# Optimization experiments

Hardware: AMD Instinct MI355X
Metric: run time of the kernel (lower is better)

Reference implementation:

```python
import jax, jax.numpy as jnp
import numpy as np

HID = 1024
OUT = 512
BATCH = 512
SEQ = 128


def setup_inputs() -> dict:
    key = jax.random.key(0)
    ks = jax.random.split(key, 8)
    s = 1.0 / np.sqrt(HID)  # PyTorch LSTM/Linear init scale
    return {
        "C": jax.random.normal(ks[0], (BATCH, HID), jnp.float32),
        "t": jax.random.uniform(ks[1], (BATCH,), jnp.float32),
        "mask": jnp.ones((SEQ, BATCH), jnp.float32),
        "W_ih": jax.random.normal(ks[2], (4 * HID, HID), jnp.float32) * s,
        "W_hh": jax.random.normal(ks[3], (4 * HID, HID), jnp.float32) * s,
        "b_ih": jax.random.normal(ks[4], (4 * HID,), jnp.float32) * s,
        "b_hh": jax.random.normal(ks[5], (4 * HID,), jnp.float32) * s,
        "W_lin": jax.random.normal(ks[6], (OUT, HID), jnp.float32) * s,
        "b_lin": jax.random.normal(ks[7], (OUT,), jnp.float32) * s,
    }


def _lstm_scan(C, W_ih, W_hh, b_ih, b_hh, seq_len):
    # Input is the same C at every step -> precompute input projection once.
    x_proj = C @ W_ih.T + b_ih + b_hh  # [B, 4H]
    B, H = C.shape

    def step(carry, _):
        h, c = carry
        gates = x_proj + h @ W_hh.T  # [B, 4H]
        i, f, g, o = jnp.split(gates, 4, axis=-1)  # PyTorch gate order i,f,g,o
        i = jax.nn.sigmoid(i)
        f = jax.nn.sigmoid(f)
        g = jnp.tanh(g)
        o = jax.nn.sigmoid(o)
        c_new = f * c + i * g
        h_new = o * jnp.tanh(c_new)
        return (h_new, c_new), h_new

    h0 = jnp.zeros((B, H), C.dtype)
    c0 = jnp.zeros((B, H), C.dtype)
    _, hs = jax.lax.scan(step, (h0, c0), None, length=seq_len)
    return hs  # [T, B, H]


def reference(C, t, mask, W_ih, W_hh, b_ih, b_hh, W_lin, b_lin):
    # t and mask are unused in the original forward (t is shadowed, mask never read).
    hs = _lstm_scan(C, W_ih, W_hh, b_ih, b_hh, SEQ)  # [T, B, H]
    out = jnp.einsum("tbh,oh->tbo", hs, W_lin) + b_lin  # [T, B, O]
    return out
```

## Files before the change

kernel.cpp:

```cpp
#include <hip/hip_runtime.h>

#define B_   512
#define H_   1024
#define G4   4096
#define OUT_ 512
#define T_   128
#define APAD 72

typedef _Float16 h8  __attribute__((ext_vector_type(8)));
typedef _Float16 h4  __attribute__((ext_vector_type(4)));
typedef float    f32x4 __attribute__((ext_vector_type(4)));

#define MFMA16(a,b,c) __builtin_amdgcn_mfma_f32_16x16x32_f16(a,b,c,0,0,0)

__device__ __forceinline__ float sigmoidf_(float x) { return 1.f / (1.f + __expf(-x)); }

__global__ __launch_bounds__(256) void setup_kernel(
    const float* __restrict__ Wih, const float* __restrict__ Whh,
    const float* __restrict__ bih, const float* __restrict__ bhh,
    const float* __restrict__ Wlin,
    _Float16* __restrict__ Wih16, _Float16* __restrict__ Whh16,
    _Float16* __restrict__ Wlin16, float* __restrict__ bsum,
    float* __restrict__ cblob, _Float16* __restrict__ h0) {
  int i = blockIdx.x * blockDim.x + threadIdx.x;
  int stride = gridDim.x * blockDim.x;
  const f32x4* wih4 = (const f32x4*)Wih;
  const f32x4* whh4 = (const f32x4*)Whh;
  h4* wih16 = (h4*)Wih16;
  h4* whh16 = (h4*)Whh16;
  f32x4 z = {};
  for (int idx = i; idx < (G4 * H_) / 4; idx += stride) {
    f32x4 a = wih4[idx], b = whh4[idx];
    h4 va, vb;
#pragma unroll
    for (int r = 0; r < 4; ++r) { va[r] = (_Float16)a[r]; vb[r] = (_Float16)b[r]; }
    wih16[idx] = va; whh16[idx] = vb;
    if (idx < (OUT_ * H_) / 4) {
      f32x4 c = ((const f32x4*)Wlin)[idx];
      h4 vc;
#pragma unroll
      for (int r = 0; r < 4; ++r) vc[r] = (_Float16)c[r];
      ((h4*)Wlin16)[idx] = vc;
      ((f32x4*)cblob)[idx] = z;
    }
    if (idx < (B_ * H_ * 2) / 16)
      ((f32x4*)h0)[idx] = z;
    if (idx < G4 / 4)
      ((f32x4*)bsum)[idx] = ((const f32x4*)bih)[idx] + ((const f32x4*)bhh)[idx];
  }
}

__device__ __forceinline__ void proj_tile(int pid,
                                          const _Float16* __restrict__ h,
                                          const _Float16* __restrict__ Wlin16,
                                          const float* __restrict__ blin,
                                          float* __restrict__ outp,
                                          _Float16* smem) {
  int m0 = (pid >> 3) * 32, n0 = (pid & 7) * 64;
  int tid = threadIdx.x, w = tid >> 6, lane = tid & 63;
  _Float16* A_s = smem;
  _Float16* B_s = smem + 32 * APAD;
  f32x4 acc[2] = {};
  int fr_row = lane & 15, fr_k = (lane >> 4) * 8;
  int ar = tid >> 3, ac = (tid & 7) * 8;
  int br = tid >> 2, bq = (tid & 3) * 16;

  for (int kt = 0; kt < 16; ++kt) {
    int k0 = kt * 64;
    *(h8*)&A_s[ar * APAD + ac] = *(const h8*)(h + (size_t)(m0 + ar) * H_ + k0 + ac);
    const _Float16* bsrc = Wlin16 + (size_t)(n0 + br) * H_ + k0 + bq;
    *(h8*)&B_s[br * APAD + bq]     = *(const h8*)bsrc;
    *(h8*)&B_s[br * APAD + bq + 8] = *(const h8*)(bsrc + 8);
    __syncthreads();
#pragma unroll
    for (int s2 = 0; s2 < 2; ++s2) {
      int ks = s2 * 32 + fr_k;
      h8 a0 = *(const h8*)&A_s[fr_row * APAD + ks];
      h8 a1 = *(const h8*)&A_s[(16 + fr_row) * APAD + ks];
      h8 b  = *(const h8*)&B_s[(w * 16 + fr_row) * APAD + ks];
      acc[0] = MFMA16(a0, b, acc[0]);
      acc[1] = MFMA16(a1, b, acc[1]);
    }
    __syncthreads();
  }
  float* fr = (float*)smem + w * 512;
  float bl = blin[n0 + w * 16 + fr_row];
#pragma unroll
  for (int mf = 0; mf < 2; ++mf)
#pragma unroll
    for (int r = 0; r < 4; ++r)
      fr[((lane >> 4) * 4 + r + mf * 16) * 16 + fr_row] = acc[mf][r] + bl;
  __syncthreads();
  int row = lane >> 2, q = (lane & 3) * 4;
#pragma unroll
  for (int p = 0; p < 2; ++p) {
    f32x4 v = *(f32x4*)&fr[(row + p * 16) * 16 + q];
    *(f32x4*)(outp + (size_t)(m0 + row + p * 16) * OUT_ + n0 + w * 16 + q) = v;
  }
}

template <int IS_XPROJ>
__global__ __launch_bounds__(256) void gates_step_kernel(
    const void* __restrict__ Ag, const _Float16* __restrict__ Wg,
    const float* __restrict__ bsum, float* __restrict__ xblob,
    float* __restrict__ cblob, _Float16* __restrict__ hout,
    const _Float16* __restrict__ Wlin16, const float* __restrict__ blin,
    float* __restrict__ outp) {
  __shared__ __align__(16) _Float16 smem[64 * APAD + 128 * APAD];

  if (!IS_XPROJ && blockIdx.x >= 256) {
    proj_tile(blockIdx.x - 256, (const _Float16*)Ag, Wlin16, blin, outp, smem);
    return;
  }

  int blk = blockIdx.x;
  int xcd = blk & 7, kq = blk >> 3;
  int j_idx = xcd * 4 + (kq & 3), m_idx = kq >> 2;
  int m0 = m_idx * 64, j0 = j_idx * 32;
  int tid = threadIdx.x, w = tid >> 6, lane = tid & 63;
  int mhalf = w >> 1, jhalf = w & 1;
  _Float16* A_s = smem;
  _Float16* B_s = smem + 64 * APAD;
  f32x4 acc[4][2] = {};
  int fr_row = lane & 15, fr_k = (lane >> 4) * 8;
  int ar = tid >> 2, ac = (tid & 3) * 16;
  int r128 = tid >> 1, bg = r128 >> 5, brr = r128 & 31, bh = (tid & 1) * 32;
  const _Float16* Brow = Wg + (size_t)(bg * H_ + j0 + brr) * H_ + bh;

  for (int kt = 0; kt < 16; ++kt) {
    int k0 = kt * 64;
    if (IS_XPROJ) {
      const float* Af = (const float*)Ag;
      const f32x4* p = (const f32x4*)(Af + (size_t)(m0 + ar) * H_ + k0 + ac);
      f32x4 v0 = p[0], v1 = p[1], v2 = p[2], v3 = p[3];
      h8 hv0, hv1;
#pragma unroll
      for (int r = 0; r < 4; ++r) {
        hv0[r] = (_Float16)v0[r]; hv0[4 + r] = (_Float16)v1[r];
        hv1[r] = (_Float16)v2[r]; hv1[4 + r] = (_Float16)v3[r];
      }
      *(h8*)&A_s[ar * APAD + ac] = hv0;
      *(h8*)&A_s[ar * APAD + ac + 8] = hv1;
    } else {
      const _Float16* Ah = (const _Float16*)Ag;
      const h8* p = (const h8*)(Ah + (size_t)(m0 + ar) * H_ + k0 + ac);
      *(h8*)&A_s[ar * APAD + ac] = p[0];
      *(h8*)&A_s[ar * APAD + ac + 8] = p[1];
    }
    {
      const h8* src = (const h8*)(Brow + k0);
      _Float16* dst = &B_s[(bg * 32 + brr) * APAD + bh];
#pragma unroll
      for (int q = 0; q < 4; ++q) *(h8*)&dst[q * 8] = src[q];
    }
    __syncthreads();
#pragma unroll
    for (int s2 = 0; s2 < 2; ++s2) {
      int ks = s2 * 32 + fr_k;
      h8 a0 = *(const h8*)&A_s[(mhalf * 32 + fr_row) * APAD + ks];
      h8 a1 = *(const h8*)&A_s[(mhalf * 32 + 16 + fr_row) * APAD + ks];
#pragma unroll
      for (int g = 0; g < 4; ++g) {
        h8 b = *(const h8*)&B_s[(g * 32 + jhalf * 16 + fr_row) * APAD + ks];
        acc[g][0] = MFMA16(a0, b, acc[g][0]);
        acc[g][1] = MFMA16(a1, b, acc[g][1]);
      }
    }
    __syncthreads();
  }

  if (IS_XPROJ) {
    f32x4* xb = (f32x4*)xblob;
#pragma unroll
    for (int g = 0; g < 4; ++g) {
      float bs = bsum[g * H_ + j0 + jhalf * 16 + fr_row];
#pragma unroll
      for (int mf = 0; mf < 2; ++mf) {
        f32x4 v = acc[g][mf];
        v += bs;
        xb[(size_t)(blk * 32 + w * 8 + g * 2 + mf) * 64 + lane] = v;
      }
    }
  } else {
    f32x4* xb = (f32x4*)xblob;
    f32x4* cb = (f32x4*)cblob;
    _Float16* hr = smem + w * 512;
#pragma unroll
    for (int mf = 0; mf < 2; ++mf) {
      f32x4 xi = xb[(size_t)(blk * 32 + w * 8 + 0 + mf) * 64 + lane];
      f32x4 xf = xb[(size_t)(blk * 32 + w * 8 + 2 + mf) * 64 + lane];
      f32x4 xg = xb[(size_t)(blk * 32 + w * 8 + 4 + mf) * 64 + lane];
      f32x4 xo = xb[(size_t)(blk * 32 + w * 8 + 6 + mf) * 64 + lane];
      f32x4 cv = cb[(size_t)(blk * 8 + w * 2 + mf) * 64 + lane];
      f32x4 cn, hn;
#pragma unroll
      for (int r = 0; r < 4; ++r) {
        float iv = sigmoidf_(acc[0][mf][r] + xi[r]);
        float fv = sigmoidf_(acc[1][mf][r] + xf[r]);
        float gv = tanhf(acc[2][mf][r] + xg[r]);
        float ov = sigmoidf_(acc[3][mf][r] + xo[r]);
        float cc = fv * cv[r] + iv * gv;
        cn[r] = cc;
        hn[r] = ov * tanhf(cc);
      }
      cb[(size_t)(blk * 8 + w * 2 + mf) * 64 + lane] = cn;
#pragma unroll
      for (int r = 0; r < 4; ++r)
        hr[((lane >> 4) * 4 + r + mf * 16) * 16 + fr_row] = (_Float16)hn[r];
    }
    __syncthreads();
    int row = lane >> 1, hb2 = (lane & 1) * 8;
    h8 hv = *(const h8*)&hr[row * 16 + hb2];
    *(h8*)(hout + (size_t)(m0 + mhalf * 32 + row) * H_ + j0 + jhalf * 16 + hb2) = hv;
  }
}

__global__ __launch_bounds__(256) void proj_kernel(const _Float16* __restrict__ h,
                                                   const _Float16* __restrict__ Wlin16,
                                                   const float* __restrict__ blin,
                                                   float* __restrict__ outp) {
  __shared__ __align__(16) _Float16 smem[64 * APAD + 128 * APAD];
  proj_tile(blockIdx.x, h, Wlin16, blin, outp, smem);
}

extern "C" void kernel_launch(void* const* d_in, const int* in_sizes, int n_in,
                              void* d_out, int out_size, void* d_ws, size_t ws_size,
                              hipStream_t stream) {
  const float* C    = (const float*)d_in[0];
  const float* Wih  = (const float*)d_in[3];
  const float* Whh  = (const float*)d_in[4];
  const float* bih  = (const float*)d_in[5];
  const float* bhh  = (const float*)d_in[6];
  const float* Wlin = (const float*)d_in[7];
  const float* blin = (const float*)d_in[8];
  float* out = (float*)d_out;

  char* ws = (char*)d_ws;
  size_t off = 0;
  auto alloc = [&](size_t bytes) {
    void* p = ws + off;
    off = (off + bytes + 255) & ~(size_t)255;
    return p;
  };
  _Float16* Wih16  = (_Float16*)alloc((size_t)G4 * H_ * 2);
  _Float16* Whh16  = (_Float16*)alloc((size_t)G4 * H_ * 2);
  _Float16* Wlin16 = (_Float16*)alloc((size_t)OUT_ * H_ * 2);
  float*    bsum   = (float*)alloc((size_t)G4 * 4);
  float*    xblob  = (float*)alloc((size_t)B_ * G4 * 4);
  float*    cblob  = (float*)alloc((size_t)B_ * H_ * 4);
  _Float16* hb0    = (_Float16*)alloc((size_t)B_ * H_ * 2);
  _Float16* hb1    = (_Float16*)alloc((size_t)B_ * H_ * 2);
  if (off > ws_size) return;

  hipLaunchKernelGGL(setup_kernel, dim3(4096), dim3(256), 0, stream,
                     Wih, Whh, bih, bhh, Wlin, Wih16, Whh16, Wlin16, bsum, cblob, hb0);

  hipLaunchKernelGGL((gates_step_kernel<1>), dim3(256), dim3(256), 0, stream,
                     (const void*)C, Wih16, bsum, xblob, (float*)nullptr,
                     (_Float16*)nullptr, (const _Float16*)nullptr,
                     (const float*)nullptr, (float*)nullptr);

  _Float16* hb[2] = {hb0, hb1};
  for (int s = 1; s <= T_; ++s) {
    const _Float16* hin = hb[(s - 1) & 1];
    _Float16* ho = hb[s & 1];
    int grid = (s >= 2) ? 384 : 256;
    float* outp = (s >= 2) ? (out + (size_t)(s - 2) * B_ * OUT_) : out;
    hipLaunchKernelGGL((gates_step_kernel<0>), dim3(grid), dim3(256), 0, stream,
                       (const void*)hin, Whh16, bsum, xblob, cblob, ho, Wlin16, blin, outp);
  }
  hipLaunchKernelGGL(proj_kernel, dim3(128), dim3(256), 0, stream,
                     hb[0], Wlin16, blin, out + (size_t)(T_ - 1) * B_ * OUT_);
}
```

Baseline: 2.533 ms.

## Replace per-step launches with persistent LSTM kernel holding W_hh in LDS

Replaces the 128 per-timestep kernel launches with a single persistent kernel of 256 blocks. Each block keeps its fp16 slice of W_hh resident in 128KB of LDS and synchronises with the others through a flag-based global barrier after each step. The input projection is folded into the persistent kernel's prologue, c stays in registers, and all hidden states are written to a full history buffer. The output projection then runs afterwards as one large double-buffered GEMM. This removes launch overhead and repeated W_hh streaming, but it relies on all 256 blocks being co-resident (otherwise the barrier deadlocks). It also adds a fast rcp-based sigmoid/tanh and a larger workspace.

```diff
diff --git a/kernel.cpp b/kernel.cpp
--- a/kernel.cpp
+++ b/kernel.cpp
@@ -2,10 +2,11 @@
 
 #define B_   512
 #define H_   1024
-#define G4   4096
 #define OUT_ 512
 #define T_   128
 #define APAD 72
+#define BUFH (192 * APAD)
+#define BH_  ((size_t)B_ * H_)
 
 typedef _Float16 h8  __attribute__((ext_vector_type(8)));
 typedef _Float16 h4  __attribute__((ext_vector_type(4)));
@@ -13,214 +14,266 @@
 
 #define MFMA16(a,b,c) __builtin_amdgcn_mfma_f32_16x16x32_f16(a,b,c,0,0,0)
 
-__device__ __forceinline__ float sigmoidf_(float x) { return 1.f / (1.f + __expf(-x)); }
-
-__global__ __launch_bounds__(256) void setup_kernel(
-    const float* __restrict__ Wih, const float* __restrict__ Whh,
-    const float* __restrict__ bih, const float* __restrict__ bhh,
-    const float* __restrict__ Wlin,
-    _Float16* __restrict__ Wih16, _Float16* __restrict__ Whh16,
-    _Float16* __restrict__ Wlin16, float* __restrict__ bsum,
-    float* __restrict__ cblob, _Float16* __restrict__ h0) {
-  int i = blockIdx.x * blockDim.x + threadIdx.x;
-  int stride = gridDim.x * blockDim.x;
-  const f32x4* wih4 = (const f32x4*)Wih;
-  const f32x4* whh4 = (const f32x4*)Whh;
-  h4* wih16 = (h4*)Wih16;
-  h4* whh16 = (h4*)Whh16;
-  f32x4 z = {};
-  for (int idx = i; idx < (G4 * H_) / 4; idx += stride) {
-    f32x4 a = wih4[idx], b = whh4[idx];
-    h4 va, vb;
-#pragma unroll
-    for (int r = 0; r < 4; ++r) { va[r] = (_Float16)a[r]; vb[r] = (_Float16)b[r]; }
-    wih16[idx] = va; whh16[idx] = vb;
-    if (idx < (OUT_ * H_) / 4) {
-      f32x4 c = ((const f32x4*)Wlin)[idx];
-      h4 vc;
-#pragma unroll
-      for (int r = 0; r < 4; ++r) vc[r] = (_Float16)c[r];
-      ((h4*)Wlin16)[idx] = vc;
-      ((f32x4*)cblob)[idx] = z;
-    }
-    if (idx < (B_ * H_ * 2) / 16)
-      ((f32x4*)h0)[idx] = z;
-    if (idx < G4 / 4)
-      ((f32x4*)bsum)[idx] = ((const f32x4*)bih)[idx] + ((const f32x4*)bhh)[idx];
-  }
-}
-
-__device__ __forceinline__ void proj_tile(int pid,
-                                          const _Float16* __restrict__ h,
-                                          const _Float16* __restrict__ Wlin16,
-                                          const float* __restrict__ blin,
-                                          float* __restrict__ outp,
-                                          _Float16* smem) {
-  int m0 = (pid >> 3) * 32, n0 = (pid & 7) * 64;
+__device__ __forceinline__ float sigf_(float x) {
+  return __builtin_amdgcn_rcpf(1.f + __expf(-x));
+}
+__device__ __forceinline__ float tanhf_(float x) {
+  x = fmaxf(fminf(x, 20.f), -20.f);
+  float e = __expf(-2.f * x);
+  return (1.f - e) * __builtin_amdgcn_rcpf(1.f + e);
+}
+__device__ __forceinline__ h8 cvt8_(f32x4 lo, f32x4 hi) {
+  h8 r;
+#pragma unroll
+  for (int e = 0; e < 4; ++e) { r[e] = (_Float16)lo[e]; r[4 + e] = (_Float16)hi[e]; }
+  return r;
+}
+
+__global__ __launch_bounds__(256) void setup2_kernel(
+    const float* __restrict__ Wlin, _Float16* __restrict__ Wlin16,
+    _Float16* __restrict__ h0) {
+  int idx = blockIdx.x * 256 + threadIdx.x;
+  f32x4 v = ((const f32x4*)Wlin)[idx];
+  h4 o;
+#pragma unroll
+  for (int r = 0; r < 4; ++r) o[r] = (_Float16)v[r];
+  ((h4*)Wlin16)[idx] = o;
+  if (idx < 65536) ((f32x4*)h0)[idx] = (f32x4){0.f, 0.f, 0.f, 0.f};
+}
+
+__device__ __forceinline__ void gridbar_(unsigned* flags, unsigned* go, unsigned gen) {
+  __syncthreads();
+  if (threadIdx.x == 0) {
+    __threadfence();
+    __hip_atomic_store(&flags[blockIdx.x], gen, __ATOMIC_RELEASE, __HIP_MEMORY_SCOPE_AGENT);
+  }
+  if (blockIdx.x == 0) {
+    while (__hip_atomic_load(&flags[threadIdx.x], __ATOMIC_ACQUIRE, __HIP_MEMORY_SCOPE_AGENT) != gen)
+      __builtin_amdgcn_s_sleep(2);
+    __syncthreads();
+    if (threadIdx.x == 0)
+      __hip_atomic_store(go, gen, __ATOMIC_RELEASE, __HIP_MEMORY_SCOPE_AGENT);
+  }
+  if (threadIdx.x == 0) {
+    while (__hip_atomic_load(go, __ATOMIC_ACQUIRE, __HIP_MEMORY_SCOPE_AGENT) != gen)
+      __builtin_amdgcn_s_sleep(4);
+    __threadfence();
+  }
+  __syncthreads();
+}
+
+__global__ __launch_bounds__(256) void lstm_persistent_kernel(
+    const float* __restrict__ C,   const float* __restrict__ Whh,
+    const float* __restrict__ Wih, const float* __restrict__ bih,
+    const float* __restrict__ bhh, _Float16* __restrict__ hs,
+    unsigned* __restrict__ flags,  unsigned* __restrict__ go) {
+  __shared__ _Float16 Wlds[64 * H_];
+
+  const int blk  = blockIdx.x;
+  const int slab = blk >> 6;
+  const int j0   = (blk & 63) * 16;
+  const int m0   = slab * 128;
+  const int tid  = threadIdx.x, w = tid >> 6, lane = tid & 63;
+  const int col  = lane & 15;
+  const int khi  = lane >> 4;
+  const int xm   = (col & 7) << 4;
+
+  f32x4 acc[4][2];
+#pragma unroll
+  for (int g = 0; g < 4; ++g) { acc[g][0] = (f32x4){0.f,0.f,0.f,0.f}; acc[g][1] = (f32x4){0.f,0.f,0.f,0.f}; }
+
+  {
+    const float* aC0 = C + (size_t)(m0 + w * 32 + col) * H_ + khi * 8;
+    const float* aC1 = aC0 + 16 * H_;
+    const float* bW0 = Wih + (size_t)(0 * H_ + j0 + col) * H_ + khi * 8;
+    const float* bW1 = Wih + (size_t)(1 * H_ + j0 + col) * H_ + khi * 8;
+    const float* bW2 = Wih + (size_t)(2 * H_ + j0 + col) * H_ + khi * 8;
+    const float* bW3 = Wih + (size_t)(3 * H_ + j0 + col) * H_ + khi * 8;
+#pragma unroll 2
+    for (int kt = 0; kt < 16; ++kt) {
+#pragma unroll
+      for (int s2 = 0; s2 < 2; ++s2) {
+        int kb = kt * 64 + s2 * 32;
+        h8 af0 = cvt8_(*(const f32x4*)(aC0 + kb), *(const f32x4*)(aC0 + kb + 4));
+        h8 af1 = cvt8_(*(const f32x4*)(aC1 + kb), *(const f32x4*)(aC1 + kb + 4));
+        h8 bf;
+        bf = cvt8_(*(const f32x4*)(bW0 + kb), *(const f32x4*)(bW0 + kb + 4));
+        acc[0][0] = MFMA16(af0, bf, acc[0][0]); acc[0][1] = MFMA16(af1, bf, acc[0][1]);
+        bf = cvt8_(*(const f32x4*)(bW1 + kb), *(const f32x4*)(bW1 + kb + 4));
+        acc[1][0] = MFMA16(af0, bf, acc[1][0]); acc[1][1] = MFMA16(af1, bf, acc[1][1]);
+        bf = cvt8_(*(const f32x4*)(bW2 + kb), *(const f32x4*)(bW2 + kb + 4));
+        acc[2][0] = MFMA16(af0, bf, acc[2][0]); acc[2][1] = MFMA16(af1, bf, acc[2][1]);
+        bf = cvt8_(*(const f32x4*)(bW3 + kb), *(const f32x4*)(bW3 + kb + 4));
+        acc[3][0] = MFMA16(af0, bf, acc[3][0]); acc[3][1] = MFMA16(af1, bf, acc[3][1]);
+      }
+    }
+  }
+  f32x4 px[4][2];
+#pragma unroll
+  for (int g = 0; g < 4; ++g) {
+    float bs = bih[g * H_ + j0 + col] + bhh[g * H_ + j0 + col];
+    px[g][0] = acc[g][0] + bs;
+    px[g][1] = acc[g][1] + bs;
+  }
+
+  {
+    int rl = tid >> 2, qc = tid & 3;
+    int grow = (rl >> 4) * H_ + j0 + (rl & 15);
+    const float* src = Whh + (size_t)grow * H_;
+    int xw = (rl & 7) << 4;
+    char* wb = (char*)Wlds + rl * 2048;
+#pragma unroll 4
+    for (int c2 = 0; c2 < 32; ++c2) {
+      int cc = qc * 32 + c2;
+      h8 v = cvt8_(*(const f32x4*)(src + cc * 8), *(const f32x4*)(src + cc * 8 + 4));
+      *(h8*)(wb + ((cc * 16) ^ xw)) = v;
+    }
+  }
+  __syncthreads();
+
+  const int arow0 = m0 + w * 32 + col;
+  f32x4 pc[2] = {(f32x4){0.f,0.f,0.f,0.f}, (f32x4){0.f,0.f,0.f,0.f}};
+  const char* wbase = (const char*)Wlds + col * 2048;
+
+#pragma unroll 1
+  for (int s = 1; s <= T_; ++s) {
+    const _Float16* hp  = hs + (size_t)(s - 1) * BH_;
+    const _Float16* ap0 = hp + (size_t)arow0 * H_ + khi * 8;
+    const _Float16* ap1 = ap0 + 16 * H_;
+#pragma unroll
+    for (int g = 0; g < 4; ++g) { acc[g][0] = (f32x4){0.f,0.f,0.f,0.f}; acc[g][1] = (f32x4){0.f,0.f,0.f,0.f}; }
+
+    h8 a[4][2][2];
+#define LDA(S, KT) do {                                                        \
+      a[S][0][0] = *(const h8*)(ap0 + (KT) * 64);                              \
+      a[S][0][1] = *(const h8*)(ap1 + (KT) * 64);                              \
+      a[S][1][0] = *(const h8*)(ap0 + (KT) * 64 + 32);                         \
+      a[S][1][1] = *(const h8*)(ap1 + (KT) * 64 + 32);                         \
+    } while (0)
+    LDA(0, 0); LDA(1, 1); LDA(2, 2);
+#pragma unroll
+    for (int kt = 0; kt < 16; ++kt) {
+      if (kt + 3 < 16) LDA((kt + 3) & 3, kt + 3);
+#pragma unroll
+      for (int s2 = 0; s2 < 2; ++s2) {
+        int boff = (kt * 128 + s2 * 64 + khi * 16) ^ xm;
+        h8 b0 = *(const h8*)(wbase + 0 * 32768 + boff);
+        h8 b1 = *(const h8*)(wbase + 1 * 32768 + boff);
+        h8 b2 = *(const h8*)(wbase + 2 * 32768 + boff);
+        h8 b3 = *(const h8*)(wbase + 3 * 32768 + boff);
+        acc[0][0] = MFMA16(a[kt & 3][s2][0], b0, acc[0][0]);
+        acc[0][1] = MFMA16(a[kt & 3][s2][1], b0, acc[0][1]);
+        acc[1][0] = MFMA16(a[kt & 3][s2][0], b1, acc[1][0]);
+        acc[1][1] = MFMA16(a[kt & 3][s2][1], b1, acc[1][1]);
+        acc[2][0] = MFMA16(a[kt & 3][s2][0], b2, acc[2][0]);
+        acc[2][1] = MFMA16(a[kt & 3][s2][1], b2, acc[2][1]);
+        acc[3][0] = MFMA16(a[kt & 3][s2][0], b3, acc[3][0]);
+        acc[3][1] = MFMA16(a[kt & 3][s2][1], b3, acc[3][1]);
+      }
+    }
+#undef LDA
+
+    _Float16* ho = hs + (size_t)s * BH_;
+#pragma unroll
+    for (int mf = 0; mf < 2; ++mf) {
+      f32x4 cn;
+#pragma unroll
+      for (int r = 0; r < 4; ++r) {
+        float iv = sigf_(acc[0][mf][r] + px[0][mf][r]);
+        float fv = sigf_(acc[1][mf][r] + px[1][mf][r]);
+        float gv = tanhf_(acc[2][mf][r] + px[2][mf][r]);
+        float ov = sigf_(acc[3][mf][r] + px[3][mf][r]);
+        float cc = fv * pc[mf][r] + iv * gv;
+        cn[r] = cc;
+        ho[(size_t)(m0 + w * 32 + mf * 16 + khi * 4 + r) * H_ + j0 + col] =
+            (_Float16)(ov * tanhf_(cc));
+      }
+      pc[mf] = cn;
+    }
+    gridbar_(flags, go, (unsigned)s);
+  }
+}
+
+__global__ __launch_bounds__(256) void proj_big_kernel(
+    const _Float16* __restrict__ h, const _Float16* __restrict__ Wlin16,
+    const float* __restrict__ blin, float* __restrict__ outp) {
+  __shared__ __align__(16) _Float16 smem[2 * BUFH];
+  int x = blockIdx.x & 7, i = blockIdx.x >> 3;
+  int mslab = x * 128 + (i >> 2);
+  int n0 = (i & 3) * 128;
+  size_t m0 = (size_t)mslab * 64;
   int tid = threadIdx.x, w = tid >> 6, lane = tid & 63;
-  _Float16* A_s = smem;
-  _Float16* B_s = smem + 32 * APAD;
-  f32x4 acc[2] = {};
-  int fr_row = lane & 15, fr_k = (lane >> 4) * 8;
-  int ar = tid >> 3, ac = (tid & 7) * 8;
-  int br = tid >> 2, bq = (tid & 3) * 16;
-
-  for (int kt = 0; kt < 16; ++kt) {
-    int k0 = kt * 64;
-    *(h8*)&A_s[ar * APAD + ac] = *(const h8*)(h + (size_t)(m0 + ar) * H_ + k0 + ac);
-    const _Float16* bsrc = Wlin16 + (size_t)(n0 + br) * H_ + k0 + bq;
-    *(h8*)&B_s[br * APAD + bq]     = *(const h8*)bsrc;
-    *(h8*)&B_s[br * APAD + bq + 8] = *(const h8*)(bsrc + 8);
-    __syncthreads();
-#pragma unroll
-    for (int s2 = 0; s2 < 2; ++s2) {
-      int ks = s2 * 32 + fr_k;
-      h8 a0 = *(const h8*)&A_s[fr_row * APAD + ks];
-      h8 a1 = *(const h8*)&A_s[(16 + fr_row) * APAD + ks];
-      h8 b  = *(const h8*)&B_s[(w * 16 + fr_row) * APAD + ks];
-      acc[0] = MFMA16(a0, b, acc[0]);
-      acc[1] = MFMA16(a1, b, acc[1]);
-    }
-    __syncthreads();
-  }
-  float* fr = (float*)smem + w * 512;
-  float bl = blin[n0 + w * 16 + fr_row];
-#pragma unroll
-  for (int mf = 0; mf < 2; ++mf)
-#pragma unroll
-    for (int r = 0; r < 4; ++r)
-      fr[((lane >> 4) * 4 + r + mf * 16) * 16 + fr_row] = acc[mf][r] + bl;
-  __syncthreads();
-  int row = lane >> 2, q = (lane & 3) * 4;
-#pragma unroll
-  for (int p = 0; p < 2; ++p) {
-    f32x4 v = *(f32x4*)&fr[(row + p * 16) * 16 + q];
-    *(f32x4*)(outp + (size_t)(m0 + row + p * 16) * OUT_ + n0 + w * 16 + q) = v;
-  }
-}
-
-template <int IS_XPROJ>
-__global__ __launch_bounds__(256) void gates_step_kernel(
-    const void* __restrict__ Ag, const _Float16* __restrict__ Wg,
-    const float* __restrict__ bsum, float* __restrict__ xblob,
-    float* __restrict__ cblob, _Float16* __restrict__ hout,
-    const _Float16* __restrict__ Wlin16, const float* __restrict__ blin,
-    float* __restrict__ outp) {
-  __shared__ __align__(16) _Float16 smem[64 * APAD + 128 * APAD];
-
-  if (!IS_XPROJ && blockIdx.x >= 256) {
-    proj_tile(blockIdx.x - 256, (const _Float16*)Ag, Wlin16, blin, outp, smem);
-    return;
-  }
-
-  int blk = blockIdx.x;
-  int xcd = blk & 7, kq = blk >> 3;
-  int j_idx = xcd * 4 + (kq & 3), m_idx = kq >> 2;
-  int m0 = m_idx * 64, j0 = j_idx * 32;
-  int tid = threadIdx.x, w = tid >> 6, lane = tid & 63;
-  int mhalf = w >> 1, jhalf = w & 1;
-  _Float16* A_s = smem;
-  _Float16* B_s = smem + 64 * APAD;
-  f32x4 acc[4][2] = {};
   int fr_row = lane & 15, fr_k = (lane >> 4) * 8;
   int ar = tid >> 2, ac = (tid & 3) * 16;
-  int r128 = tid >> 1, bg = r128 >> 5, brr = r128 & 31, bh = (tid & 1) * 32;
-  const _Float16* Brow = Wg + (size_t)(bg * H_ + j0 + brr) * H_ + bh;
-
+  int br = tid >> 1, bq = (tid & 1) * 32;
+  const _Float16* Arow = h + (m0 + ar) * H_ + ac;
+  const _Float16* Brow = Wlin16 + (size_t)(n0 + br) * H_ + bq;
+  f32x4 acc[4][2] = {};
+  h8 ra0, ra1, rb0, rb1, rb2, rb3;
+
+#define LOADP(K0) do {                                                        \
+    const h8* pa_ = (const h8*)(Arow + (K0));                                 \
+    ra0 = pa_[0]; ra1 = pa_[1];                                               \
+    const h8* pb_ = (const h8*)(Brow + (K0));                                 \
+    rb0 = pb_[0]; rb1 = pb_[1]; rb2 = pb_[2]; rb3 = pb_[3];                   \
+  } while (0)
+#define STOREP(BUF) do {                                                      \
+    _Float16* As_ = smem + (BUF) * BUFH;                                      \
+    _Float16* Bs_ = As_ + 64 * APAD;                                          \
+    *(h8*)&As_[ar * APAD + ac] = ra0;                                         \
+    *(h8*)&As_[ar * APAD + ac + 8] = ra1;                                     \
+    _Float16* dst_ = &Bs_[br * APAD + bq];                                    \
+    *(h8*)&dst_[0] = rb0; *(h8*)&dst_[8] = rb1;                               \
+    *(h8*)&dst_[16] = rb2; *(h8*)&dst_[24] = rb3;                             \
+  } while (0)
+#define COMPUTEP(BUF) do {                                                    \
+    const _Float16* As_ = smem + (BUF) * BUFH;                                \
+    const _Float16* Bs_ = As_ + 64 * APAD;                                    \
+    _Pragma("unroll")                                                         \
+    for (int s2 = 0; s2 < 2; ++s2) {                                          \
+      int ks = s2 * 32 + fr_k;                                                \
+      h8 b0 = *(const h8*)&Bs_[(w * 32 + fr_row) * APAD + ks];                \
+      h8 b1 = *(const h8*)&Bs_[(w * 32 + 16 + fr_row) * APAD + ks];           \
+      _Pragma("unroll")                                                       \
+      for (int mf = 0; mf < 4; ++mf) {                                        \
+        h8 a = *(const h8*)&As_[(mf * 16 + fr_row) * APAD + ks];              \
+        acc[mf][0] = MFMA16(a, b0, acc[mf][0]);                               \
+        acc[mf][1] = MFMA16(a, b1, acc[mf][1]);                               \
+      }                                                                       \
+    }                                                                         \
+  } while (0)
+
+  LOADP(0);
+  STOREP(0);
+  __syncthreads();
+#pragma unroll
   for (int kt = 0; kt < 16; ++kt) {
-    int k0 = kt * 64;
-    if (IS_XPROJ) {
-      const float* Af = (const float*)Ag;
-      const f32x4* p = (const f32x4*)(Af + (size_t)(m0 + ar) * H_ + k0 + ac);
-      f32x4 v0 = p[0], v1 = p[1], v2 = p[2], v3 = p[3];
-      h8 hv0, hv1;
-#pragma unroll
-      for (int r = 0; r < 4; ++r) {
-        hv0[r] = (_Float16)v0[r]; hv0[4 + r] = (_Float16)v1[r];
-        hv1[r] = (_Float16)v2[r]; hv1[4 + r] = (_Float16)v3[r];
-      }
-      *(h8*)&A_s[ar * APAD + ac] = hv0;
-      *(h8*)&A_s[ar * APAD + ac + 8] = hv1;
-    } else {
-      const _Float16* Ah = (const _Float16*)Ag;
-      const h8* p = (const h8*)(Ah + (size_t)(m0 + ar) * H_ + k0 + ac);
-      *(h8*)&A_s[ar * APAD + ac] = p[0];
-      *(h8*)&A_s[ar * APAD + ac + 8] = p[1];
-    }
-    {
-      const h8* src = (const h8*)(Brow + k0);
-      _Float16* dst = &B_s[(bg * 32 + brr) * APAD + bh];
-#pragma unroll
-      for (int q = 0; q < 4; ++q) *(h8*)&dst[q * 8] = src[q];
-    }
+    if (kt < 15) LOADP((kt + 1) * 64);
+    COMPUTEP(kt & 1);
+    if (kt < 15) STOREP((kt + 1) & 1);
     __syncthreads();
-#pragma unroll
-    for (int s2 = 0; s2 < 2; ++s2) {
-      int ks = s2 * 32 + fr_k;
-      h8 a0 = *(const h8*)&A_s[(mhalf * 32 + fr_row) * APAD + ks];
-      h8 a1 = *(const h8*)&A_s[(mhalf * 32 + 16 + fr_row) * APAD + ks];
-#pragma unroll
-      for (int g = 0; g < 4; ++g) {
-        h8 b = *(const h8*)&B_s[(g * 32 + jhalf * 16 + fr_row) * APAD + ks];
-        acc[g][0] = MFMA16(a0, b, acc[g][0]);
-        acc[g][1] = MFMA16(a1, b, acc[g][1]);
-      }
-    }
-    __syncthreads();
-  }
-
-  if (IS_XPROJ) {
-    f32x4* xb = (f32x4*)xblob;
-#pragma unroll
-    for (int g = 0; g < 4; ++g) {
-      float bs = bsum[g * H_ + j0 + jhalf * 16 + fr_row];
-#pragma unroll
-      for (int mf = 0; mf < 2; ++mf) {
-        f32x4 v = acc[g][mf];
-        v += bs;
-        xb[(size_t)(blk * 32 + w * 8 + g * 2 + mf) * 64 + lane] = v;
-      }
-    }
-  } else {
-    f32x4* xb = (f32x4*)xblob;
-    f32x4* cb = (f32x4*)cblob;
-    _Float16* hr = smem + w * 512;
-#pragma unroll
-    for (int mf = 0; mf < 2; ++mf) {
-      f32x4 xi = xb[(size_t)(blk * 32 + w * 8 + 0 + mf) * 64 + lane];
-      f32x4 xf = xb[(size_t)(blk * 32 + w * 8 + 2 + mf) * 64 + lane];
-      f32x4 xg = xb[(size_t)(blk * 32 + w * 8 + 4 + mf) * 64 + lane];
-      f32x4 xo = xb[(size_t)(blk * 32 + w * 8 + 6 + mf) * 64 + lane];
-      f32x4 cv = cb[(size_t)(blk * 8 + w * 2 + mf) * 64 + lane];
-      f32x4 cn, hn;
-#pragma unroll
-      for (int r = 0; r < 4; ++r) {
-        float iv = sigmoidf_(acc[0][mf][r] + xi[r]);
-        float fv = sigmoidf_(acc[1][mf][r] + xf[r]);
-        float gv = tanhf(acc[2][mf][r] + xg[r]);
-        float ov = sigmoidf_(acc[3][mf][r] + xo[r]);
-        float cc = fv * cv[r] + iv * gv;
-        cn[r] = cc;
-        hn[r] = ov * tanhf(cc);
-      }
-      cb[(size_t)(blk * 8 + w * 2 + mf) * 64 + lane] = cn;
-#pragma unroll
-      for (int r = 0; r < 4; ++r)
-        hr[((lane >> 4) * 4 + r + mf * 16) * 16 + fr_row] = (_Float16)hn[r];
-    }
-    __syncthreads();
-    int row = lane >> 1, hb2 = (lane & 1) * 8;
-    h8 hv = *(const h8*)&hr[row * 16 + hb2];
-    *(h8*)(hout + (size_t)(m0 + mhalf * 32 + row) * H_ + j0 + jhalf * 16 + hb2) = hv;
-  }
-}
-
-__global__ __launch_bounds__(256) void proj_kernel(const _Float16* __restrict__ h,
-                                                   const _Float16* __restrict__ Wlin16,
-                                                   const float* __restrict__ blin,
-                                                   float* __restrict__ outp) {
-  __shared__ __align__(16) _Float16 smem[64 * APAD + 128 * APAD];
-  proj_tile(blockIdx.x, h, Wlin16, blin, outp, smem);
+  }
+#undef LOADP
+#undef STOREP
+#undef COMPUTEP
+
+  float* fr = (float*)smem + w * 2048;
+  float bl0 = blin[n0 + w * 32 + fr_row];
+  float bl1 = blin[n0 + w * 32 + 16 + fr_row];
+#pragma unroll
+  for (int mf = 0; mf < 4; ++mf)
+#pragma unroll
+    for (int r = 0; r < 4; ++r) {
+      fr[(mf * 16 + (lane >> 4) * 4 + r) * 32 + fr_row]      = acc[mf][0][r] + bl0;
+      fr[(mf * 16 + (lane >> 4) * 4 + r) * 32 + 16 + fr_row] = acc[mf][1][r] + bl1;
+    }
+  __syncthreads();
+#pragma unroll
+  for (int p = 0; p < 8; ++p) {
+    int row = p * 8 + (lane >> 3), q = (lane & 7) * 4;
+    f32x4 v = *(f32x4*)&fr[row * 32 + q];
+    *(f32x4*)(outp + (m0 + row) * OUT_ + n0 + w * 32 + q) = v;
+  }
 }
 
 extern "C" void kernel_launch(void* const* d_in, const int* in_sizes, int n_in,
@@ -242,33 +295,16 @@
     off = (off + bytes + 255) & ~(size_t)255;
     return p;
   };
-  _Float16* Wih16  = (_Float16*)alloc((size_t)G4 * H_ * 2);
-  _Float16* Whh16  = (_Float16*)alloc((size_t)G4 * H_ * 2);
   _Float16* Wlin16 = (_Float16*)alloc((size_t)OUT_ * H_ * 2);
-  float*    bsum   = (float*)alloc((size_t)G4 * 4);
-  float*    xblob  = (float*)alloc((size_t)B_ * G4 * 4);
-  float*    cblob  = (float*)alloc((size_t)B_ * H_ * 4);
-  _Float16* hb0    = (_Float16*)alloc((size_t)B_ * H_ * 2);
-  _Float16* hb1    = (_Float16*)alloc((size_t)B_ * H_ * 2);
+  _Float16* hs     = (_Float16*)alloc((size_t)(T_ + 1) * BH_ * 2);
+  unsigned* flags  = (unsigned*)alloc(256 * sizeof(unsigned));
+  unsigned* go     = (unsigned*)alloc(256);
   if (off > ws_size) return;
 
-  hipLaunchKernelGGL(setup_kernel, dim3(4096), dim3(256), 0, stream,
-                     Wih, Whh, bih, bhh, Wlin, Wih16, Whh16, Wlin16, bsum, cblob, hb0);
-
-  hipLaunchKernelGGL((gates_step_kernel<1>), dim3(256), dim3(256), 0, stream,
-                     (const void*)C, Wih16, bsum, xblob, (float*)nullptr,
-                     (_Float16*)nullptr, (const _Float16*)nullptr,
-                     (const float*)nullptr, (float*)nullptr);
-
-  _Float16* hb[2] = {hb0, hb1};
-  for (int s = 1; s <= T_; ++s) {
-    const _Float16* hin = hb[(s - 1) & 1];
-    _Float16* ho = hb[s & 1];
-    int grid = (s >= 2) ? 384 : 256;
-    float* outp = (s >= 2) ? (out + (size_t)(s - 2) * B_ * OUT_) : out;
-    hipLaunchKernelGGL((gates_step_kernel<0>), dim3(grid), dim3(256), 0, stream,
-                       (const void*)hin, Whh16, bsum, xblob, cblob, ho, Wlin16, blin, outp);
-  }
-  hipLaunchKernelGGL(proj_kernel, dim3(128), dim3(256), 0, stream,
-                     hb[0], Wlin16, blin, out + (size_t)(T_ - 1) * B_ * OUT_);
-}
+  hipLaunchKernelGGL(setup2_kernel, dim3(512), dim3(256), 0, stream,
+                     Wlin, Wlin16, hs );
+  hipLaunchKernelGGL(lstm_persistent_kernel, dim3(256), dim3(256), 0, stream,
+                     C, Whh, Wih, bih, bhh, hs, flags, go);
+  hipLaunchKernelGGL(proj_big_kernel, dim3((T_ * B_ / 64) * (OUT_ / 128)),
+                     dim3(256), 0, stream, hs + BH_, Wlin16, blin, out);
+}
```

New measurement: 5.102 ms. 101% more time.
